# Kernel tuning notes

Hardware: AMD Instinct MI355X
Metric: run time of the kernel (lower is better)

## Reference

```python
import jax, jax.numpy as jnp
import numpy as np

N, H, V, K = 2048, 1024, 50304, 16
C = V // K  # tokens per POS cluster


def setup_inputs() -> dict:
    key = jax.random.key(0)
    kx, ky, kw, kl = jax.random.split(key, 4)
    x = jax.random.normal(kx, (N, H), dtype=jnp.float32)
    y = jax.random.randint(ky, (N,), 0, V, dtype=jnp.int32)
    # consistent POS label: token y belongs to cluster y // C
    y_pos = (y // C).astype(jnp.int32)
    # pos2token[i] = token ids of cluster i (equal contiguous partition)
    pos2token = jnp.arange(V, dtype=jnp.int32).reshape(K, C)
    # token_in_pos_id[i][v] = within-cluster index of token v in cluster i
    token_in_pos_id = jnp.broadcast_to(jnp.arange(V, dtype=jnp.int32) % C, (K, V))
    cluster_w = jax.random.normal(kw, (H, K), dtype=jnp.float32) * 0.02
    logits = jax.random.normal(kl, (H, V), dtype=jnp.float32) * 0.02
    return {"x": x, "y": y, "y_pos": y_pos, "pos2token": pos2token,
            "token_in_pos_id": token_in_pos_id, "cluster_w": cluster_w, "logits": logits}


def reference(x, y, y_pos, pos2token, token_in_pos_id, cluster_w, logits):
    # cluster (POS) log-probs: [N, K]
    cluster_ll = jax.nn.log_softmax(x @ cluster_w, axis=1)
    # per-cluster weight slices gathered once: [H, K, C]
    W = logits[:, pos2token.reshape(-1)].reshape(H, K, C)
    # tail logits for every token against every cluster's token set: [N, K, C]
    tail_lp = jax.nn.log_softmax(jnp.einsum('nh,hkc->nkc', x, W), axis=-1)
    n = jnp.arange(y.shape[0])
    within = token_in_pos_id[y_pos, y]          # within-cluster target id
    nll = -cluster_ll[n, y_pos] - tail_lp[n, y_pos, within]
    return nll
```

## Files before the change

### kernel.cpp

```cpp
#include <hip/hip_runtime.h>
#include <hip/hip_bf16.h>

#define NROW 2048
#define HDIM 1024
#define VOC  50304
#define KCL  16
#define CDIM 3144

#define MT 128
#define NT 128
#define BK 32
#define PK 36

#define WS_SUMEXP 0
#define WS_COUNTS 2048
#define WS_PART   2064
#define WS_ZTGT   4112
#define WS_TCOL   6160
#define WS_ROWS   8208

typedef __attribute__((ext_vector_type(8))) short short8;
typedef __attribute__((ext_vector_type(4))) short short4v;
typedef __attribute__((ext_vector_type(4))) float f32x4;

__device__ __forceinline__ ushort2 f2bf2(float a, float b) {
    union { __hip_bfloat162 h; ushort2 u; } cv;
    cv.h = __float22bfloat162_rn(float2{a, b});
    return cv.u;
}

__global__ void scatter_kernel(const int* __restrict__ y,
                               const int* __restrict__ y_pos,
                               const int* __restrict__ tip,
                               int* ws_i) {
    int n = blockIdx.x * 256 + threadIdx.x;
    if (n >= NROW) return;
    int kn = y_pos[n];
    int slot = atomicAdd(&ws_i[WS_COUNTS + kn], 1);
    ws_i[WS_ROWS + kn * NROW + slot] = n;
    ws_i[WS_TCOL + n] = tip[kn * VOC + y[n]];
}

__global__ void cluster_kernel(const float* __restrict__ x,
                               const float* __restrict__ cw,
                               const int* __restrict__ y_pos,
                               float* ws_f) {
    int wave = threadIdx.x >> 6;
    int lane = threadIdx.x & 63;
    int n = blockIdx.x * 4 + wave;
    float acc[KCL];
#pragma unroll
    for (int k = 0; k < KCL; k++) acc[k] = 0.f;
#pragma unroll
    for (int j = 0; j < 16; j++) {
        int h = j * 64 + lane;
        float xv = x[(size_t)n * HDIM + h];
        const float4* cwr = (const float4*)(cw + (size_t)h * KCL);
#pragma unroll
        for (int q = 0; q < 4; q++) {
            float4 w = cwr[q];
            acc[q * 4 + 0] += xv * w.x;
            acc[q * 4 + 1] += xv * w.y;
            acc[q * 4 + 2] += xv * w.z;
            acc[q * 4 + 3] += xv * w.w;
        }
    }
#pragma unroll
    for (int off = 32; off >= 1; off >>= 1) {
#pragma unroll
        for (int k = 0; k < KCL; k++) acc[k] += __shfl_down(acc[k], off);
    }
    if (lane == 0) {
        int kn = y_pos[n];
        float m = acc[0];
#pragma unroll
        for (int k = 1; k < KCL; k++) m = fmaxf(m, acc[k]);
        float s = 0.f;
        float skn = 0.f;
#pragma unroll
        for (int k = 0; k < KCL; k++) {
            s += __expf(acc[k] - m);
            skn = (k == kn) ? acc[k] : skn;
        }
        ws_f[WS_PART + n] = (m + __logf(s)) - skn;
    }
}

__launch_bounds__(256, 2)
__global__ void tail_kernel(const float* __restrict__ x,
                            const float* __restrict__ logits,
                            const int* ws_i, float* ws_f) {
    __shared__ short As[MT * PK];
    __shared__ short Bs[NT * PK];
    __shared__ int   lrow[MT];
    __shared__ int   ltcol[MT];
    __shared__ float rowsum[MT];

    const int k  = blockIdx.y;
    const int ct = blockIdx.x;
    const int rt = blockIdx.z;
    const int Mk = ws_i[WS_COUNTS + k];
    if (rt * MT >= Mk) return;

    const int tid = threadIdx.x;
    if (tid < MT) {
        int r = rt * MT + tid;
        int rid = (r < Mk) ? ws_i[WS_ROWS + k * NROW + r] : -1;
        lrow[tid]  = rid;
        ltcol[tid] = (rid >= 0) ? ws_i[WS_TCOL + rid] : -1;
        rowsum[tid] = 0.f;
    }
    __syncthreads();

    const int ai = tid >> 1;
    const int ah = (tid & 1) * 16;
    const int aRow = lrow[ai];
    const int bn  = tid & 127;
    const int bk0 = (tid >> 7) * 16;
    const int clB = ct * NT + bn;
    const int gcol = k * CDIM + ((clB < CDIM) ? clB : (CDIM - 1));

    const int w    = tid >> 6;
    const int l    = tid & 63;
    const int wr   = (w >> 1) * 64;
    const int wc   = (w & 1) * 64;
    const int quad = l >> 4;
    const int lm   = l & 15;

    f32x4 acc[4][4];
#pragma unroll
    for (int mi = 0; mi < 4; mi++)
#pragma unroll
        for (int ni = 0; ni < 4; ni++) acc[mi][ni] = (f32x4)(0.f);

    union frag_u { short4v s4[2]; short8 s8; };
    union stage_u { ushort2 u2[8]; short4v s4[4]; };

    for (int h0 = 0; h0 < HDIM; h0 += BK) {
        {
            stage_u ta;
            if (aRow >= 0) {
                const float4* src = (const float4*)(x + (size_t)aRow * HDIM + h0 + ah);
#pragma unroll
                for (int q = 0; q < 4; q++) {
                    float4 v = src[q];
                    ta.u2[q * 2 + 0] = f2bf2(v.x, v.y);
                    ta.u2[q * 2 + 1] = f2bf2(v.z, v.w);
                }
            } else {
#pragma unroll
                for (int q = 0; q < 8; q++) ta.u2[q] = ushort2{0, 0};
            }
            short4v* dst = (short4v*)&As[ai * PK + ah];
#pragma unroll
            for (int q = 0; q < 4; q++) dst[q] = ta.s4[q];
        }
        {
            stage_u tb;
            const float* bp = logits + (size_t)(h0 + bk0) * VOC + gcol;
#pragma unroll
            for (int j = 0; j < 8; j++) {
                float v0 = bp[(size_t)(2 * j) * VOC];
                float v1 = bp[(size_t)(2 * j + 1) * VOC];
                tb.u2[j] = f2bf2(v0, v1);
            }
            short4v* dst = (short4v*)&Bs[bn * PK + bk0];
#pragma unroll
            for (int q = 0; q < 4; q++) dst[q] = tb.s4[q];
        }
        __syncthreads();

        short8 a[4], b[4];
#pragma unroll
        for (int mi = 0; mi < 4; mi++) {
            frag_u f;
            const short4v* p = (const short4v*)&As[(wr + mi * 16 + lm) * PK + quad * 8];
            f.s4[0] = p[0]; f.s4[1] = p[1];
            a[mi] = f.s8;
        }
#pragma unroll
        for (int ni = 0; ni < 4; ni++) {
            frag_u f;
            const short4v* p = (const short4v*)&Bs[(wc + ni * 16 + lm) * PK + quad * 8];
            f.s4[0] = p[0]; f.s4[1] = p[1];
            b[ni] = f.s8;
        }
#pragma unroll
        for (int mi = 0; mi < 4; mi++)
#pragma unroll
            for (int ni = 0; ni < 4; ni++)
                acc[mi][ni] = __builtin_amdgcn_mfma_f32_16x16x32_bf16(
                    a[mi], b[ni], acc[mi][ni], 0, 0, 0);
        __syncthreads();
    }

#pragma unroll
    for (int mi = 0; mi < 4; mi++) {
#pragma unroll
        for (int r = 0; r < 4; r++) {
            int row_local = wr + mi * 16 + quad * 4 + r;
            int rid = lrow[row_local];
            int tc  = ltcol[row_local];
            float s = 0.f;
#pragma unroll
            for (int ni = 0; ni < 4; ni++) {
                int cl = ct * NT + wc + ni * 16 + lm;
                float z = acc[mi][ni][r];
                if (rid >= 0 && cl < CDIM) {
                    s += __expf(z);
                    if (cl == tc) ws_f[WS_ZTGT + rid] = z;
                }
            }
            s += __shfl_xor(s, 1);
            s += __shfl_xor(s, 2);
            s += __shfl_xor(s, 4);
            s += __shfl_xor(s, 8);
            if (lm == 0 && rid >= 0) atomicAdd(&rowsum[row_local], s);
        }
    }
    __syncthreads();
    if (tid < MT) {
        int rid = lrow[tid];
        if (rid >= 0) atomicAdd(&ws_f[WS_SUMEXP + rid], rowsum[tid]);
    }
}

__global__ void finalize_kernel(const float* ws_f, float* __restrict__ out) {
    int n = blockIdx.x * 256 + threadIdx.x;
    if (n >= NROW) return;
    out[n] = ws_f[WS_PART + n] + __logf(ws_f[WS_SUMEXP + n]) - ws_f[WS_ZTGT + n];
}

extern "C" void kernel_launch(void* const* d_in, const int* in_sizes, int n_in,
                              void* d_out, int out_size, void* d_ws, size_t ws_size,
                              hipStream_t stream) {
    const float* x      = (const float*)d_in[0];
    const int*   y      = (const int*)d_in[1];
    const int*   y_pos  = (const int*)d_in[2];
    const int*   tip    = (const int*)d_in[4];
    const float* cw     = (const float*)d_in[5];
    const float* logits = (const float*)d_in[6];
    float* out  = (float*)d_out;
    float* ws_f = (float*)d_ws;
    int*   ws_i = (int*)d_ws;

    hipMemsetAsync(d_ws, 0, (size_t)(NROW + KCL) * 4, stream);

    scatter_kernel<<<NROW / 256, 256, 0, stream>>>(y, y_pos, tip, ws_i);
    cluster_kernel<<<NROW / 4, 256, 0, stream>>>(x, cw, y_pos, ws_f);

    dim3 grid((CDIM + NT - 1) / NT, KCL, NROW / MT);
    tail_kernel<<<grid, 256, 0, stream>>>(x, logits, ws_i, ws_f);

    finalize_kernel<<<NROW / 256, 256, 0, stream>>>(ws_f, out);
}
```

Baseline: 345.0 us.

## Pre-gather bf16 x rows per cluster and stream A tiles via global_load_lds

A prep kernel now converts each cluster's gathered x rows to bf16 once, stores them in a zero-padded workspace with a fixed per-cluster capacity, and also computes the cluster log-softmax. The tail kernel loads A tiles straight into LDS with global_load_lds, so the GEMM no longer re-gathers and re-converts x from fp32. B loads now use float2 reads into a permuted unpadded LDS layout. The fixed capacity of 256 rows per cluster assumes balanced clusters; rows beyond it would be silently dropped, and the tail grid is now sized by CAP rather than NROW.

```diff
diff --git a/kernel.cpp b/kernel.cpp
--- a/kernel.cpp
+++ b/kernel.cpp
@@ -10,7 +10,7 @@
 #define MT 128
 #define NT 128
 #define BK 32
-#define PK 36
+#define CAP 256
 
 #define WS_SUMEXP 0
 #define WS_COUNTS 2048
@@ -18,6 +18,7 @@
 #define WS_ZTGT   4112
 #define WS_TCOL   6160
 #define WS_ROWS   8208
+#define WS_XG     40976
 
 typedef __attribute__((ext_vector_type(8))) short short8;
 typedef __attribute__((ext_vector_type(4))) short short4v;
@@ -27,6 +28,16 @@
     union { __hip_bfloat162 h; ushort2 u; } cv;
     cv.h = __float22bfloat162_rn(float2{a, b});
     return cv.u;
+}
+
+__device__ __forceinline__ void gload_lds16(const void* g, void* l) {
+    const uint32_t __attribute__((address_space(1)))* gp =
+        reinterpret_cast<const uint32_t __attribute__((address_space(1)))*>(
+            reinterpret_cast<uintptr_t>(g));
+    uint32_t __attribute__((address_space(3)))* lp =
+        reinterpret_cast<uint32_t __attribute__((address_space(3)))*>(
+            static_cast<uint32_t>(reinterpret_cast<uintptr_t>(l)));
+    __builtin_amdgcn_global_load_lds(gp, lp, 16, 0, 0);
 }
 
 __global__ void scatter_kernel(const int* __restrict__ y,
@@ -41,57 +52,76 @@
     ws_i[WS_TCOL + n] = tip[kn * VOC + y[n]];
 }
 
-__global__ void cluster_kernel(const float* __restrict__ x,
-                               const float* __restrict__ cw,
-                               const int* __restrict__ y_pos,
-                               float* ws_f) {
-    int wave = threadIdx.x >> 6;
-    int lane = threadIdx.x & 63;
-    int n = blockIdx.x * 4 + wave;
+__global__ void prep_kernel(const float* __restrict__ x,
+                            const float* __restrict__ cw,
+                            const int* __restrict__ ws_i, float* ws_f) {
+    const int wave = threadIdx.x >> 6;
+    const int lane = threadIdx.x & 63;
+    const int gw = blockIdx.x * 4 + wave;
+    const int k = gw >> 8;
+    const int slot = gw & (CAP - 1);
+    const int Mk = ws_i[WS_COUNTS + k];
+    short4v* dst = (short4v*)((const short*)(ws_i + WS_XG) + ((size_t)gw << 10));
+    if (slot >= Mk) {
+        short4v z = {0, 0, 0, 0};
+#pragma unroll
+        for (int q = 0; q < 4; q++) dst[q * 64 + lane] = z;
+        return;
+    }
+    const int n = ws_i[WS_ROWS + k * NROW + slot];
+    const float4* xr = (const float4*)(x + (size_t)n * HDIM);
+    float4 v[4];
+#pragma unroll
+    for (int q = 0; q < 4; q++) v[q] = xr[q * 64 + lane];
+#pragma unroll
+    for (int q = 0; q < 4; q++) {
+        union { ushort2 u2[2]; short4v s4; } t;
+        t.u2[0] = f2bf2(v[q].x, v[q].y);
+        t.u2[1] = f2bf2(v[q].z, v[q].w);
+        dst[q * 64 + lane] = t.s4;
+    }
     float acc[KCL];
 #pragma unroll
-    for (int k = 0; k < KCL; k++) acc[k] = 0.f;
-#pragma unroll
-    for (int j = 0; j < 16; j++) {
-        int h = j * 64 + lane;
-        float xv = x[(size_t)n * HDIM + h];
-        const float4* cwr = (const float4*)(cw + (size_t)h * KCL);
-#pragma unroll
-        for (int q = 0; q < 4; q++) {
-            float4 w = cwr[q];
-            acc[q * 4 + 0] += xv * w.x;
-            acc[q * 4 + 1] += xv * w.y;
-            acc[q * 4 + 2] += xv * w.z;
-            acc[q * 4 + 3] += xv * w.w;
+    for (int kk = 0; kk < KCL; kk++) acc[kk] = 0.f;
+#pragma unroll
+    for (int q = 0; q < 4; q++) {
+        const float* vf = (const float*)&v[q];
+#pragma unroll
+        for (int e = 0; e < 4; e++) {
+            const int h = q * 256 + lane * 4 + e;
+            const float xv = vf[e];
+            const float4* cwr = (const float4*)(cw + (size_t)h * KCL);
+#pragma unroll
+            for (int qq = 0; qq < 4; qq++) {
+                float4 w = cwr[qq];
+                acc[qq * 4 + 0] += xv * w.x;
+                acc[qq * 4 + 1] += xv * w.y;
+                acc[qq * 4 + 2] += xv * w.z;
+                acc[qq * 4 + 3] += xv * w.w;
+            }
         }
     }
 #pragma unroll
     for (int off = 32; off >= 1; off >>= 1) {
 #pragma unroll
-        for (int k = 0; k < KCL; k++) acc[k] += __shfl_down(acc[k], off);
+        for (int kk = 0; kk < KCL; kk++) acc[kk] += __shfl_down(acc[kk], off);
     }
     if (lane == 0) {
-        int kn = y_pos[n];
         float m = acc[0];
 #pragma unroll
-        for (int k = 1; k < KCL; k++) m = fmaxf(m, acc[k]);
+        for (int kk = 1; kk < KCL; kk++) m = fmaxf(m, acc[kk]);
         float s = 0.f;
-        float skn = 0.f;
-#pragma unroll
-        for (int k = 0; k < KCL; k++) {
-            s += __expf(acc[k] - m);
-            skn = (k == kn) ? acc[k] : skn;
-        }
-        ws_f[WS_PART + n] = (m + __logf(s)) - skn;
+#pragma unroll
+        for (int kk = 0; kk < KCL; kk++) s += __expf(acc[kk] - m);
+        ws_f[WS_PART + n] = (m + __logf(s)) - acc[k];
     }
 }
 
 __launch_bounds__(256, 2)
-__global__ void tail_kernel(const float* __restrict__ x,
-                            const float* __restrict__ logits,
+__global__ void tail_kernel(const float* __restrict__ logits,
                             const int* ws_i, float* ws_f) {
-    __shared__ short As[MT * PK];
-    __shared__ short Bs[NT * PK];
+    __shared__ __align__(16) short As[4 * MT * 8];
+    __shared__ __align__(16) short Bs[4 * NT * 8];
     __shared__ int   lrow[MT];
     __shared__ int   ltcol[MT];
     __shared__ float rowsum[MT];
@@ -110,18 +140,19 @@
         ltcol[tid] = (rid >= 0) ? ws_i[WS_TCOL + rid] : -1;
         rowsum[tid] = 0.f;
     }
-    __syncthreads();
-
-    const int ai = tid >> 1;
-    const int ah = (tid & 1) * 16;
-    const int aRow = lrow[ai];
-    const int bn  = tid & 127;
-    const int bk0 = (tid >> 7) * 16;
-    const int clB = ct * NT + bn;
-    const int gcol = k * CDIM + ((clB < CDIM) ? clB : (CDIM - 1));
-
-    const int w    = tid >> 6;
-    const int l    = tid & 63;
+
+    const short* xg = (const short*)(ws_i + WS_XG)
+                    + ((size_t)(k * CAP + rt * MT) << 10);
+    const int row0 = tid & 127;
+    const int k80  = tid >> 7;
+    const short* xrow = xg + (size_t)row0 * HDIM;
+
+    const int w  = tid >> 6;
+    const int l  = tid & 63;
+    const int col0 = ct * NT + 2 * l;
+    const int cp   = (col0 <= CDIM - 2) ? col0 : (CDIM - 2);
+    const float* bp = logits + (size_t)(w * 8) * VOC + (k * CDIM + cp);
+
     const int wr   = (w >> 1) * 64;
     const int wc   = (w & 1) * 64;
     const int quad = l >> 4;
@@ -133,57 +164,38 @@
 #pragma unroll
         for (int ni = 0; ni < 4; ni++) acc[mi][ni] = (f32x4)(0.f);
 
-    union frag_u { short4v s4[2]; short8 s8; };
-    union stage_u { ushort2 u2[8]; short4v s4[4]; };
+    __syncthreads();
 
     for (int h0 = 0; h0 < HDIM; h0 += BK) {
+        gload_lds16(xrow + (k80 * 8) + h0,       &As[(size_t)tid * 8]);
+        gload_lds16(xrow + ((k80 + 2) * 8) + h0, &As[(size_t)(256 + tid) * 8]);
+
         {
-            stage_u ta;
-            if (aRow >= 0) {
-                const float4* src = (const float4*)(x + (size_t)aRow * HDIM + h0 + ah);
-#pragma unroll
-                for (int q = 0; q < 4; q++) {
-                    float4 v = src[q];
-                    ta.u2[q * 2 + 0] = f2bf2(v.x, v.y);
-                    ta.u2[q * 2 + 1] = f2bf2(v.z, v.w);
-                }
-            } else {
-#pragma unroll
-                for (int q = 0; q < 8; q++) ta.u2[q] = ushort2{0, 0};
+            float2 bv[8];
+            const float* bpp = bp + (size_t)h0 * VOC;
+#pragma unroll
+            for (int j = 0; j < 8; j++)
+                bv[j] = *(const float2*)(bpp + (size_t)j * VOC);
+            union { ushort2 u2[4]; short8 s8; } ue, uo;
+#pragma unroll
+            for (int t = 0; t < 4; t++) {
+                ue.u2[t] = f2bf2(bv[2 * t].x, bv[2 * t + 1].x);
+                uo.u2[t] = f2bf2(bv[2 * t].y, bv[2 * t + 1].y);
             }
-            short4v* dst = (short4v*)&As[ai * PK + ah];
-#pragma unroll
-            for (int q = 0; q < 4; q++) dst[q] = ta.s4[q];
-        }
-        {
-            stage_u tb;
-            const float* bp = logits + (size_t)(h0 + bk0) * VOC + gcol;
-#pragma unroll
-            for (int j = 0; j < 8; j++) {
-                float v0 = bp[(size_t)(2 * j) * VOC];
-                float v1 = bp[(size_t)(2 * j + 1) * VOC];
-                tb.u2[j] = f2bf2(v0, v1);
-            }
-            short4v* dst = (short4v*)&Bs[bn * PK + bk0];
-#pragma unroll
-            for (int q = 0; q < 4; q++) dst[q] = tb.s4[q];
+            *(short8*)&Bs[(size_t)(w * 128 + l) * 8]      = ue.s8;
+            *(short8*)&Bs[(size_t)(w * 128 + 64 + l) * 8] = uo.s8;
         }
         __syncthreads();
 
         short8 a[4], b[4];
 #pragma unroll
-        for (int mi = 0; mi < 4; mi++) {
-            frag_u f;
-            const short4v* p = (const short4v*)&As[(wr + mi * 16 + lm) * PK + quad * 8];
-            f.s4[0] = p[0]; f.s4[1] = p[1];
-            a[mi] = f.s8;
-        }
+        for (int mi = 0; mi < 4; mi++)
+            a[mi] = *(const short8*)&As[(size_t)(quad * 128 + wr + mi * 16 + lm) * 8];
 #pragma unroll
         for (int ni = 0; ni < 4; ni++) {
-            frag_u f;
-            const short4v* p = (const short4v*)&Bs[(wc + ni * 16 + lm) * PK + quad * 8];
-            f.s4[0] = p[0]; f.s4[1] = p[1];
-            b[ni] = f.s8;
+            int C = wc + ni * 16 + lm;
+            int cperm = (C >> 1) | ((C & 1) << 6);
+            b[ni] = *(const short8*)&Bs[(size_t)(quad * 128 + cperm) * 8];
         }
 #pragma unroll
         for (int mi = 0; mi < 4; mi++)
@@ -247,10 +259,10 @@
     hipMemsetAsync(d_ws, 0, (size_t)(NROW + KCL) * 4, stream);
 
     scatter_kernel<<<NROW / 256, 256, 0, stream>>>(y, y_pos, tip, ws_i);
-    cluster_kernel<<<NROW / 4, 256, 0, stream>>>(x, cw, y_pos, ws_f);
-
-    dim3 grid((CDIM + NT - 1) / NT, KCL, NROW / MT);
-    tail_kernel<<<grid, 256, 0, stream>>>(x, logits, ws_i, ws_f);
+    prep_kernel<<<KCL * CAP / 4, 256, 0, stream>>>(x, cw, ws_i, ws_f);
+
+    dim3 grid((CDIM + NT - 1) / NT, KCL, CAP / MT);
+    tail_kernel<<<grid, 256, 0, stream>>>(logits, ws_i, ws_f);
 
     finalize_kernel<<<NROW / 256, 256, 0, stream>>>(ws_f, out);
 }
```

Result: slower. 383.8 us (+11.2%).
